# Optimization experiments

Measured on AMD Instinct MI355X. Metric: run time of the kernel, lower is better.

The kernel has to match this reference:

```python
import jax, jax.numpy as jnp
import numpy as np

D_MODEL = 2048
N_HEADS = 16
N_KV_HEADS = 4
DH = D_MODEL // N_HEADS          # 128
GROUPS = N_HEADS // N_KV_HEADS   # 4
ROPE_BASE = 10000.0
B, T = 2, 2048


def _rope_tables(positions):
    # positions: [T] int -> cos,sin [T, DH//2]
    inv = 1.0 / (ROPE_BASE ** (jnp.arange(0, DH, 2, dtype=jnp.float32) / DH))
    ang = positions.astype(jnp.float32)[:, None] * inv[None, :]
    return jnp.cos(ang), jnp.sin(ang)


def _apply_rope(x, cos, sin):
    # x: [B,H,T,DH]; cos/sin: [1,1,T,DH//2]; interleaved even/odd rotation
    even, odd = x[..., ::2], x[..., 1::2]
    xe = even * cos - odd * sin
    xo = even * sin + odd * cos
    return jnp.stack([xe, xo], axis=-1).reshape(x.shape)


def setup_inputs() -> dict:
    key = jax.random.key(0)
    k1, k2, k3 = jax.random.split(key, 3)
    qkv_dim = D_MODEL + 2 * N_KV_HEADS * DH
    x = jax.random.normal(k1, (B, T, D_MODEL), dtype=jnp.float32)
    Wqkv = jax.random.normal(k2, (D_MODEL, qkv_dim), dtype=jnp.float32) / np.sqrt(D_MODEL).astype(np.float32)
    Wo = jax.random.normal(k3, (N_HEADS * DH, D_MODEL), dtype=jnp.float32) / np.sqrt(N_HEADS * DH).astype(np.float32)
    return {"x": x, "Wqkv": Wqkv, "Wo": Wo, "start_pos": 0}


def reference(x, Wqkv, Wo, start_pos):
    Bx, Tx, _ = x.shape
    qkv = x @ Wqkv  # [B,T,D + 2*HKV*DH]
    q, k, v = jnp.split(qkv, [N_HEADS * DH, N_HEADS * DH + N_KV_HEADS * DH], axis=-1)
    q = q.reshape(Bx, Tx, N_HEADS, DH).transpose(0, 2, 1, 3)      # [B,H,T,DH]
    k = k.reshape(Bx, Tx, N_KV_HEADS, DH).transpose(0, 2, 1, 3)   # [B,HKV,T,DH]
    v = v.reshape(Bx, Tx, N_KV_HEADS, DH).transpose(0, 2, 1, 3)

    pos = start_pos + jnp.arange(Tx)
    cos, sin = _rope_tables(pos)
    cos = cos[None, None]; sin = sin[None, None]
    q = _apply_rope(q, cos, sin)
    k = _apply_rope(k, cos, sin)

    # GQA: repeat_interleave kv heads
    k = jnp.repeat(k, GROUPS, axis=1)  # [B,H,T,DH]
    v = jnp.repeat(v, GROUPS, axis=1)

    scale = 1.0 / np.sqrt(DH).astype(np.float32)
    att = jnp.einsum('bhqd,bhkd->bhqk', q, k) * scale
    causal = jnp.triu(jnp.ones((Tx, Tx), dtype=bool), 1)
    att = jnp.where(causal[None, None], jnp.float32(-jnp.inf), att)
    att = jax.nn.softmax(att, axis=-1)
    y = jnp.einsum('bhqk,bhkd->bhqd', att, v)
    y = y.transpose(0, 2, 1, 3).reshape(Bx, Tx, N_HEADS * DH)
    return y @ Wo
```

## Files before the change

kernel.cpp:

```cpp
#include <hip/hip_runtime.h>
#include <math.h>

#define D_MODEL 2048
#define N_HEADS 16
#define N_KV    4
#define DH      128
#define QKV_DIM 3072
#define TT      2048
#define BB      2
#define ROWS    (BB*TT)

#define VS_STRIDE 72
#define PS_STRIDE 72

typedef unsigned short u16;
typedef short short8 __attribute__((ext_vector_type(8)));
typedef short short4v __attribute__((ext_vector_type(4)));
typedef float float4v __attribute__((ext_vector_type(4)));

__device__ inline float b2f(u16 h) {
    union { unsigned u; float f; } v; v.u = ((unsigned)h) << 16; return v.f;
}
__device__ inline u16 f2b(float f) {
    union { float f; unsigned u; } v; v.f = f;
    unsigned r = v.u + 0x7FFF + ((v.u >> 16) & 1);
    return (u16)(r >> 16);
}

__device__ inline void async16(const void* g, void* l) {
    __builtin_amdgcn_global_load_lds(
        (const __attribute__((address_space(1))) void*)g,
        (__attribute__((address_space(3))) void*)l, 16, 0, 0);
}

__global__ void convert_f2b(const float* __restrict__ src, u16* __restrict__ dst) {
    int i = blockIdx.x * 256 + threadIdx.x;
    float4v a = *(const float4v*)(src + (size_t)i * 4);
    short4v p;
    p[0] = (short)f2b(a[0]); p[1] = (short)f2b(a[1]);
    p[2] = (short)f2b(a[2]); p[3] = (short)f2b(a[3]);
    *(short4v*)(dst + (size_t)i * 4) = p;
}

__global__ void transpose_f2b(const float* __restrict__ src, u16* __restrict__ dst,
                              int R, int C, int col0) {
    __shared__ __align__(16) u16 tile[32][33];
    int bc = blockIdx.x * 32, br = blockIdx.y * 32;
    int tx = threadIdx.x & 31, ty = threadIdx.x >> 5;
    for (int i = ty; i < 32; i += 8)
        tile[i][tx] = f2b(src[(size_t)(br + i) * C + col0 + bc + tx]);
    __syncthreads();
    for (int i = ty; i < 32; i += 8)
        dst[(size_t)(bc + i) * R + br + tx] = tile[tx][i];
}

template<bool F32OUT, bool ROPE>
__global__ __launch_bounds__(256) void gemm_bt_async(
    const u16* __restrict__ A, const u16* __restrict__ Bt1, const u16* __restrict__ Bt2,
    int nsplit, void* __restrict__ Cv, int M, int N, int K, const int* __restrict__ sp) {
    __shared__ __align__(16) u16 As[128 * 32];
    __shared__ __align__(16) u16 Bs[128 * 32];
    const int tid = threadIdx.x;
    const int wave = tid >> 6, lane = tid & 63;
    const int quad = lane >> 4, l16 = lane & 15;
    const int bm = blockIdx.y * 128, bn = blockIdx.x * 128;
    const int wm = (wave >> 1) * 64, wn = (wave & 1) * 64;
    const int srow = wave * 32 + (lane >> 2);
    const int scol = (lane & 3) * 8;
    const u16* Bt = (bn < nsplit) ? (Bt1 + (size_t)bn * K)
                                  : (Bt2 + (size_t)(bn - nsplit) * K);

    float4v acc[4][4] = {};

    for (int k0 = 0; k0 < K; k0 += 32) {
        async16(A + (size_t)(bm + srow) * K + k0 + scol, (char*)As + wave * 2048);
        async16(A + (size_t)(bm + srow + 16) * K + k0 + scol, (char*)As + wave * 2048 + 1024);
        async16(Bt + (size_t)srow * K + k0 + scol, (char*)Bs + wave * 2048);
        async16(Bt + (size_t)(srow + 16) * K + k0 + scol, (char*)Bs + wave * 2048 + 1024);
        __syncthreads();
        short8 af[4], bf[4];
#pragma unroll
        for (int i = 0; i < 4; i++)
            af[i] = *(const short8*)(As + (wm + i * 16 + l16) * 32 + quad * 8);
#pragma unroll
        for (int j = 0; j < 4; j++)
            bf[j] = *(const short8*)(Bs + (wn + j * 16 + l16) * 32 + quad * 8);
#pragma unroll
        for (int i = 0; i < 4; i++)
#pragma unroll
            for (int j = 0; j < 4; j++)
                acc[i][j] = __builtin_amdgcn_mfma_f32_16x16x32_bf16(af[i], bf[j], acc[i][j], 0, 0, 0);
        __syncthreads();
    }
    const int sp0 = ROPE ? *sp : 0;
#pragma unroll
    for (int j = 0; j < 4; j++) {
        int col = bn + wn + j * 16 + l16;
        bool do_rope = ROPE && (col < 2560);
        float inv = 0.f;
        if (do_rope) inv = __expf(-0.14391156816f * (float)((col & 127) >> 1));
#pragma unroll
        for (int i = 0; i < 4; i++) {
            int row0 = bm + wm + i * 16 + quad * 4;
#pragma unroll
            for (int r = 0; r < 4; r++) {
                float v = acc[i][j][r];
                if (do_rope) {
                    float partner = __shfl_xor(v, 1, 64);
                    float ang = (float)(sp0 + ((row0 + r) & (TT - 1))) * inv;
                    float c = __cosf(ang), s = __sinf(ang);
                    v = (col & 1) ? (partner * s + v * c)
                                  : (v * c - partner * s);
                }
                if (F32OUT) ((float*)Cv)[(size_t)(row0 + r) * N + col] = v;
                else        ((u16*)Cv)[(size_t)(row0 + r) * N + col] = f2b(v);
            }
        }
    }
}

__global__ __launch_bounds__(512) void attn_kernel(
    const u16* __restrict__ qkv, u16* __restrict__ y) {
    __shared__ __align__(16) u16 Ks[2][64 * 128];
    __shared__ __align__(16) u16 Vs[128 * VS_STRIDE];
    __shared__ __align__(16) u16 Ps[8][16 * PS_STRIDE];

    const int tid = threadIdx.x;
    const int wave = tid >> 6, lane = tid & 63;
    const int quad = lane >> 4, l16 = lane & 15;
    const int bx = blockIdx.x;
    const int xg = bx & 7;
    const int b = xg >> 2, hk = xg & 3;
    const int jj = bx >> 3;
    const int h = hk * 4 + (jj & 3);
    const int qq = jj >> 2;
    const int qt = (qq & 1) ? (15 - (qq >> 1)) : (qq >> 1);
    const int qcol = h * 128;
    const int kcol = 2048 + hk * 128;
    const int vcol = 2560 + hk * 128;
    const float scale = 0.08838834764831845f;

    const int wq0 = qt * 128 + wave * 16;
    const u16* qrow = qkv + (size_t)(b * TT + wq0 + l16) * QKV_DIM + qcol;
    short8 qf[4];
#pragma unroll
    for (int d = 0; d < 4; d++)
        qf[d] = *(const short8*)(qrow + d * 32 + quad * 8);

    float4v Oacc[9] = {};
    const short8 ONES = {(short)0x3F80, (short)0x3F80, (short)0x3F80, (short)0x3F80,
                         (short)0x3F80, (short)0x3F80, (short)0x3F80, (short)0x3F80};

    const int ktmax = 2 * qt + 1;

    size_t kg[2];
#pragma unroll
    for (int s = 0; s < 2; s++) {
        int rl = s * 4 + (lane >> 4);
        kg[s] = (size_t)(wave * 8 + rl) * QKV_DIM + (size_t)(((lane & 15) ^ rl) * 8);
    }
    {
        const u16* kb = qkv + (size_t)(b * TT) * QKV_DIM + kcol;
        async16(kb + kg[0], (char*)Ks[0] + wave * 2048);
        async16(kb + kg[1], (char*)Ks[0] + wave * 2048 + 1024);
    }
    short8 vreg[2];
#pragma unroll
    for (int s = 0; s < 2; s++)
        vreg[s] = *(const short8*)(qkv + (size_t)(b * TT + lane) * QKV_DIM + vcol + (wave * 2 + s) * 8);

    for (int kt = 0; kt <= ktmax; kt++) {
        const u16* Kcur = Ks[kt & 1];
        __syncthreads();
#pragma unroll
        for (int s = 0; s < 2; s++) {
            int dgi = wave * 2 + s;
#pragma unroll
            for (int j8 = 0; j8 < 8; j8++)
                Vs[(dgi * 8 + j8) * VS_STRIDE + lane] = (u16)vreg[s][j8];
        }
        __syncthreads();
        if (kt < ktmax) {
            const u16* kb = qkv + (size_t)(b * TT + (kt + 1) * 64) * QKV_DIM;
            async16(kb + kcol + kg[0], (char*)Ks[(kt + 1) & 1] + wave * 2048);
            async16(kb + kcol + kg[1], (char*)Ks[(kt + 1) & 1] + wave * 2048 + 1024);
#pragma unroll
            for (int s = 0; s < 2; s++)
                vreg[s] = *(const short8*)(kb + (size_t)lane * QKV_DIM + vcol + (wave * 2 + s) * 8);
        }

        float4v S[4] = {};
#pragma unroll
        for (int d = 0; d < 4; d++) {
#pragma unroll
            for (int j = 0; j < 4; j++) {
                short8 bk = *(const short8*)(Kcur + (j * 16 + l16) * 128
                                             + (((d * 4 + quad) ^ (l16 & 7)) * 8));
                S[j] = __builtin_amdgcn_mfma_f32_16x16x32_bf16(qf[d], bk, S[j], 0, 0, 0);
            }
        }
        const int qbase = wq0 + quad * 4;
        const int kvb = kt * 64 + l16;
        const bool diag = (kt * 64 + 63 > wq0);
#pragma unroll
        for (int j = 0; j < 4; j++)
#pragma unroll
            for (int r = 0; r < 4; r++) {
                bool masked = diag && (kvb + j * 16 > qbase + r);
                float p = masked ? 0.f : __expf(S[j][r] * scale);
                Ps[wave][(quad * 4 + r) * PS_STRIDE + j * 16 + l16] = f2b(p);
            }
        __asm__ volatile("s_waitcnt lgkmcnt(0)" ::: "memory");
#pragma unroll
        for (int ks = 0; ks < 2; ks++) {
            short8 ap = *(const short8*)(Ps[wave] + l16 * PS_STRIDE + ks * 32 + quad * 8);
#pragma unroll
            for (int dt = 0; dt < 8; dt++) {
                short8 bv = *(const short8*)(Vs + (dt * 16 + l16) * VS_STRIDE + ks * 32 + quad * 8);
                Oacc[dt] = __builtin_amdgcn_mfma_f32_16x16x32_bf16(ap, bv, Oacc[dt], 0, 0, 0);
            }
            Oacc[8] = __builtin_amdgcn_mfma_f32_16x16x32_bf16(ap, ONES, Oacc[8], 0, 0, 0);
        }
    }
#pragma unroll
    for (int dt = 0; dt < 8; dt++)
#pragma unroll
        for (int r = 0; r < 4; r++) {
            float v = Oacc[dt][r] / Oacc[8][r];
            y[(size_t)(b * TT + wq0 + quad * 4 + r) * D_MODEL
              + h * 128 + dt * 16 + l16] = f2b(v);
        }
}

extern "C" void kernel_launch(void* const* d_in, const int* in_sizes, int n_in,
                              void* d_out, int out_size, void* d_ws, size_t ws_size,
                              hipStream_t stream) {
    const float* x    = (const float*)d_in[0];
    const float* Wqkv = (const float*)d_in[1];
    const float* Wo   = (const float*)d_in[2];
    const int*   sp   = (const int*)d_in[3];

    char* ws = (char*)d_ws;
    char* dob = (char*)d_out;
    u16*   xb     = (u16*)ws;
    u16*   Y      = (u16*)ws;
    u16*   WqkvTA = (u16*)(ws + 16777216);
    u16*   WoT    = (u16*)(ws + 16777216);
    u16*   QKV    = (u16*)d_out;
    u16*   WqkvTB = (u16*)(dob + 25165824);
    float* out    = (float*)d_out;

    convert_f2b<<<ROWS * D_MODEL / 4 / 256, 256, 0, stream>>>(x, xb);
    transpose_f2b<<<dim3(64, 64), 256, 0, stream>>>(Wqkv, WqkvTA, D_MODEL, QKV_DIM, 0);
    transpose_f2b<<<dim3(32, 64), 256, 0, stream>>>(Wqkv, WqkvTB, D_MODEL, QKV_DIM, 2048);
    gemm_bt_async<false, true><<<dim3(QKV_DIM / 128, ROWS / 128), 256, 0, stream>>>(
        xb, WqkvTA, WqkvTB, 2048, QKV, ROWS, QKV_DIM, D_MODEL, sp);
    transpose_f2b<<<dim3(64, 64), 256, 0, stream>>>(Wo, WoT, D_MODEL, D_MODEL, 0);
    attn_kernel<<<512, 512, 0, stream>>>(QKV, Y);
    gemm_bt_async<true, false><<<dim3(D_MODEL / 128, ROWS / 128), 256, 0, stream>>>(
        Y, WoT, WoT, D_MODEL, out, ROWS, D_MODEL, D_MODEL, sp);
}
```

Measured before the change: 350.9 us.

## Give each attention wave two 16-row query groups to reuse K/V fragments

The attention kernel now runs 4 waves of 256 threads instead of 8, and each wave handles 32 query rows split into two 16-row MFMA groups. Each K and V fragment read from LDS now feeds two MFMAs, which halves LDS read traffic per FLOP, and the per-block K/V staging loads are spread over fewer threads. The q-tile schedule also changes from alternating short/long tiles to a mirrored order. The cost is higher register pressure (double accumulators), fewer waves per block to hide latency, and a launch bound that asks for 2 blocks per SIMD.

```diff
diff --git a/kernel.cpp b/kernel.cpp
--- a/kernel.cpp
+++ b/kernel.cpp
@@ -119,11 +119,11 @@
     }
 }
 
-__global__ __launch_bounds__(512) void attn_kernel(
+__global__ __launch_bounds__(256, 2) void attn_kernel(
     const u16* __restrict__ qkv, u16* __restrict__ y) {
     __shared__ __align__(16) u16 Ks[2][64 * 128];
     __shared__ __align__(16) u16 Vs[128 * VS_STRIDE];
-    __shared__ __align__(16) u16 Ps[8][16 * PS_STRIDE];
+    __shared__ __align__(16) u16 Ps[4][32 * PS_STRIDE];
 
     const int tid = threadIdx.x;
     const int wave = tid >> 6, lane = tid & 63;
@@ -134,47 +134,53 @@
     const int jj = bx >> 3;
     const int h = hk * 4 + (jj & 3);
     const int qq = jj >> 2;
-    const int qt = (qq & 1) ? (15 - (qq >> 1)) : (qq >> 1);
+    const int qt = (qq < 8) ? qq : (23 - qq);
     const int qcol = h * 128;
     const int kcol = 2048 + hk * 128;
     const int vcol = 2560 + hk * 128;
     const float scale = 0.08838834764831845f;
 
-    const int wq0 = qt * 128 + wave * 16;
-    const u16* qrow = qkv + (size_t)(b * TT + wq0 + l16) * QKV_DIM + qcol;
-    short8 qf[4];
-#pragma unroll
-    for (int d = 0; d < 4; d++)
-        qf[d] = *(const short8*)(qrow + d * 32 + quad * 8);
-
-    float4v Oacc[9] = {};
+    const int wq0 = qt * 128 + wave * 32;
+    short8 qf[2][4];
+#pragma unroll
+    for (int g = 0; g < 2; g++) {
+        const u16* qrow = qkv + (size_t)(b * TT + wq0 + g * 16 + l16) * QKV_DIM + qcol;
+#pragma unroll
+        for (int d = 0; d < 4; d++)
+            qf[g][d] = *(const short8*)(qrow + d * 32 + quad * 8);
+    }
+
+    float4v Oacc[2][8] = {};
+    float4v Ol[2] = {};
     const short8 ONES = {(short)0x3F80, (short)0x3F80, (short)0x3F80, (short)0x3F80,
                          (short)0x3F80, (short)0x3F80, (short)0x3F80, (short)0x3F80};
 
     const int ktmax = 2 * qt + 1;
 
-    size_t kg[2];
-#pragma unroll
-    for (int s = 0; s < 2; s++) {
-        int rl = s * 4 + (lane >> 4);
-        kg[s] = (size_t)(wave * 8 + rl) * QKV_DIM + (size_t)(((lane & 15) ^ rl) * 8);
+    size_t kg[4];
+#pragma unroll
+    for (int s = 0; s < 4; s++) {
+        int rl = (s * 4 + quad) & 7;
+        kg[s] = (size_t)(wave * 16 + s * 4 + quad) * QKV_DIM
+              + (size_t)((l16 ^ rl) * 8);
     }
     {
-        const u16* kb = qkv + (size_t)(b * TT) * QKV_DIM + kcol;
-        async16(kb + kg[0], (char*)Ks[0] + wave * 2048);
-        async16(kb + kg[1], (char*)Ks[0] + wave * 2048 + 1024);
-    }
-    short8 vreg[2];
-#pragma unroll
-    for (int s = 0; s < 2; s++)
-        vreg[s] = *(const short8*)(qkv + (size_t)(b * TT + lane) * QKV_DIM + vcol + (wave * 2 + s) * 8);
+        const u16* kb = qkv + (size_t)(b * TT) * QKV_DIM;
+#pragma unroll
+        for (int s = 0; s < 4; s++)
+            async16(kb + kcol + kg[s], (char*)Ks[0] + wave * 4096 + s * 1024);
+    }
+    short8 vreg[4];
+#pragma unroll
+    for (int s = 0; s < 4; s++)
+        vreg[s] = *(const short8*)(qkv + (size_t)(b * TT + lane) * QKV_DIM + vcol + (wave * 4 + s) * 8);
 
     for (int kt = 0; kt <= ktmax; kt++) {
         const u16* Kcur = Ks[kt & 1];
         __syncthreads();
 #pragma unroll
-        for (int s = 0; s < 2; s++) {
-            int dgi = wave * 2 + s;
+        for (int s = 0; s < 4; s++) {
+            int dgi = wave * 4 + s;
 #pragma unroll
             for (int j8 = 0; j8 < 8; j8++)
                 Vs[(dgi * 8 + j8) * VS_STRIDE + lane] = (u16)vreg[s][j8];
@@ -182,54 +188,69 @@
         __syncthreads();
         if (kt < ktmax) {
             const u16* kb = qkv + (size_t)(b * TT + (kt + 1) * 64) * QKV_DIM;
-            async16(kb + kcol + kg[0], (char*)Ks[(kt + 1) & 1] + wave * 2048);
-            async16(kb + kcol + kg[1], (char*)Ks[(kt + 1) & 1] + wave * 2048 + 1024);
-#pragma unroll
-            for (int s = 0; s < 2; s++)
-                vreg[s] = *(const short8*)(kb + (size_t)lane * QKV_DIM + vcol + (wave * 2 + s) * 8);
-        }
-
-        float4v S[4] = {};
+#pragma unroll
+            for (int s = 0; s < 4; s++)
+                async16(kb + kcol + kg[s], (char*)Ks[(kt + 1) & 1] + wave * 4096 + s * 1024);
+#pragma unroll
+            for (int s = 0; s < 4; s++)
+                vreg[s] = *(const short8*)(kb + (size_t)lane * QKV_DIM + vcol + (wave * 4 + s) * 8);
+        }
+
+        float4v S[2][4] = {};
 #pragma unroll
         for (int d = 0; d < 4; d++) {
 #pragma unroll
             for (int j = 0; j < 4; j++) {
                 short8 bk = *(const short8*)(Kcur + (j * 16 + l16) * 128
                                              + (((d * 4 + quad) ^ (l16 & 7)) * 8));
-                S[j] = __builtin_amdgcn_mfma_f32_16x16x32_bf16(qf[d], bk, S[j], 0, 0, 0);
-            }
-        }
-        const int qbase = wq0 + quad * 4;
+#pragma unroll
+                for (int g = 0; g < 2; g++)
+                    S[g][j] = __builtin_amdgcn_mfma_f32_16x16x32_bf16(qf[g][d], bk, S[g][j], 0, 0, 0);
+            }
+        }
         const int kvb = kt * 64 + l16;
         const bool diag = (kt * 64 + 63 > wq0);
 #pragma unroll
-        for (int j = 0; j < 4; j++)
-#pragma unroll
-            for (int r = 0; r < 4; r++) {
-                bool masked = diag && (kvb + j * 16 > qbase + r);
-                float p = masked ? 0.f : __expf(S[j][r] * scale);
-                Ps[wave][(quad * 4 + r) * PS_STRIDE + j * 16 + l16] = f2b(p);
-            }
+        for (int g = 0; g < 2; g++) {
+            const int qbase = wq0 + g * 16 + quad * 4;
+#pragma unroll
+            for (int j = 0; j < 4; j++)
+#pragma unroll
+                for (int r = 0; r < 4; r++) {
+                    bool masked = diag && (kvb + j * 16 > qbase + r);
+                    float p = masked ? 0.f : __expf(S[g][j][r] * scale);
+                    Ps[wave][(g * 16 + quad * 4 + r) * PS_STRIDE + j * 16 + l16] = f2b(p);
+                }
+        }
         __asm__ volatile("s_waitcnt lgkmcnt(0)" ::: "memory");
 #pragma unroll
         for (int ks = 0; ks < 2; ks++) {
-            short8 ap = *(const short8*)(Ps[wave] + l16 * PS_STRIDE + ks * 32 + quad * 8);
+            short8 ap[2];
+#pragma unroll
+            for (int g = 0; g < 2; g++)
+                ap[g] = *(const short8*)(Ps[wave] + (g * 16 + l16) * PS_STRIDE + ks * 32 + quad * 8);
 #pragma unroll
             for (int dt = 0; dt < 8; dt++) {
                 short8 bv = *(const short8*)(Vs + (dt * 16 + l16) * VS_STRIDE + ks * 32 + quad * 8);
-                Oacc[dt] = __builtin_amdgcn_mfma_f32_16x16x32_bf16(ap, bv, Oacc[dt], 0, 0, 0);
-            }
-            Oacc[8] = __builtin_amdgcn_mfma_f32_16x16x32_bf16(ap, ONES, Oacc[8], 0, 0, 0);
-        }
-    }
-#pragma unroll
-    for (int dt = 0; dt < 8; dt++)
-#pragma unroll
-        for (int r = 0; r < 4; r++) {
-            float v = Oacc[dt][r] / Oacc[8][r];
-            y[(size_t)(b * TT + wq0 + quad * 4 + r) * D_MODEL
-              + h * 128 + dt * 16 + l16] = f2b(v);
-        }
+#pragma unroll
+                for (int g = 0; g < 2; g++)
+                    Oacc[g][dt] = __builtin_amdgcn_mfma_f32_16x16x32_bf16(ap[g], bv, Oacc[g][dt], 0, 0, 0);
+            }
+#pragma unroll
+            for (int g = 0; g < 2; g++)
+                Ol[g] = __builtin_amdgcn_mfma_f32_16x16x32_bf16(ap[g], ONES, Ol[g], 0, 0, 0);
+        }
+    }
+#pragma unroll
+    for (int g = 0; g < 2; g++)
+#pragma unroll
+        for (int dt = 0; dt < 8; dt++)
+#pragma unroll
+            for (int r = 0; r < 4; r++) {
+                float v = Oacc[g][dt][r] / Ol[g][r];
+                y[(size_t)(b * TT + wq0 + g * 16 + quad * 4 + r) * D_MODEL
+                  + h * 128 + dt * 16 + l16] = f2b(v);
+            }
 }
 
 extern "C" void kernel_launch(void* const* d_in, const int* in_sizes, int n_in,
@@ -256,7 +277,7 @@
     gemm_bt_async<false, true><<<dim3(QKV_DIM / 128, ROWS / 128), 256, 0, stream>>>(
         xb, WqkvTA, WqkvTB, 2048, QKV, ROWS, QKV_DIM, D_MODEL, sp);
     transpose_f2b<<<dim3(64, 64), 256, 0, stream>>>(Wo, WoT, D_MODEL, D_MODEL, 0);
-    attn_kernel<<<512, 512, 0, stream>>>(QKV, Y);
+    attn_kernel<<<512, 256, 0, stream>>>(QKV, Y);
     gemm_bt_async<true, false><<<dim3(D_MODEL / 128, ROWS / 128), 256, 0, stream>>>(
         Y, WoT, WoT, D_MODEL, out, ROWS, D_MODEL, D_MODEL, sp);
 }
```

After: 353.9 us. No clear change (+0.9%).
